# Optimization experiments

Hardware: AMD Instinct MI355X
Metric: run time of the kernel (lower is better)

The kernel has to match this reference:

```python
import jax, jax.numpy as jnp
import numpy as np

N = 131072      # packets
KD = 128        # key_dim
DM = 256        # d_model
HD = 256        # hidden_dim
NC = 1024       # num_compute_nodes
AD = 64         # address_dim
SCALE = 0.1     # residual_scale
ROLE_WRITER = 0


def _ln(x, g, b, eps=1e-5):
    m = jnp.mean(x, axis=-1, keepdims=True)
    v = jnp.mean((x - m) ** 2, axis=-1, keepdims=True)
    return (x - m) * jax.lax.rsqrt(v + eps) * g + b


def setup_inputs() -> dict:
    key = jax.random.key(0)
    ks = jax.random.split(key, 16)
    f32 = jnp.float32

    def w(k, shape):
        return jax.random.normal(k, shape, dtype=f32) * 0.02

    inp = {
        "routing_key": jax.random.normal(ks[0], (N, KD), f32),
        "aux_features": jax.random.normal(ks[1], (N, DM), f32),
        "residual": jax.random.normal(ks[2], (N, DM), f32),
        "role": jax.random.randint(ks[3], (N,), 0, 3, dtype=jnp.int32),
        # input projections
        "Wk": w(ks[4], (KD, HD)), "bk": jnp.zeros((HD,), f32),
        "Wa": w(ks[5], (DM, HD)), "ba": jnp.zeros((HD,), f32),
        "Wr": w(ks[6], (DM, HD)), "br": jnp.zeros((HD,), f32),
        # input layernorm
        "g_in": jnp.ones((HD,), f32), "b_in": jnp.zeros((HD,), f32),
        # backbone layer 0 (Linear + GELU + LN)
        "Wb0": w(ks[7], (HD, HD)), "bb0": jnp.zeros((HD,), f32),
        "g0": jnp.ones((HD,), f32), "beta0": jnp.zeros((HD,), f32),
        # backbone layer 1
        "Wb1": w(ks[8], (HD, HD)), "bb1": jnp.zeros((HD,), f32),
        "g1": jnp.ones((HD,), f32), "beta1": jnp.zeros((HD,), f32),
        # role-specific heads
        "Ww": w(ks[9], (HD, NC)), "bw": jnp.zeros((NC,), f32),
        "Wq": w(ks[10], (HD, NC)), "bq": jnp.zeros((NC,), f32),
        # address head (aux_type == 'address_l2')
        "Wad": w(ks[11], (HD, AD)), "bad": jnp.zeros((AD,), f32),
    }
    return inp


def reference(routing_key, aux_features, residual, role,
              Wk, bk, Wa, ba, Wr, br, g_in, b_in,
              Wb0, bb0, g0, beta0, Wb1, bb1, g1, beta1,
              Ww, bw, Wq, bq, Wad, bad):
    # hidden = key_proj(key) + aux_proj(aux) + scale * residual_proj(residual)
    h = (routing_key @ Wk + bk) + (aux_features @ Wa + ba) \
        + SCALE * (residual @ Wr + br)
    h = _ln(h, g_in, b_in)
    # backbone: [Linear -> GELU -> LN] x layers
    for W, bL, g, be in ((Wb0, bb0, g0, beta0), (Wb1, bb1, g1, beta1)):
        h = _ln(jax.nn.gelu(h @ W + bL, approximate=False), g, be)
    # role-masked head dispatch: writers use writer_head; query + other rows
    # use query_head (matches the torch masked gather/scatter semantics)
    writer = (role == ROLE_WRITER)[:, None]
    logits = jnp.where(writer, h @ Ww + bw, h @ Wq + bq)
    aux_address = h @ Wad + bad
    return logits, h, aux_address
```

## Files before the change

kernel.cpp:

```cpp
#include <hip/hip_runtime.h>
#include <hip/hip_bf16.h>

#define N_PKT 131072
#define KD 128
#define DM 256
#define HDIM 256
#define NCOMP 1024
#define ADIM 64

typedef __attribute__((ext_vector_type(8))) short v8s;
typedef __attribute__((ext_vector_type(4))) float v4f;

__device__ inline unsigned short f2bf(float f) {
  __hip_bfloat16 h = __float2bfloat16(f);
  return *reinterpret_cast<unsigned short*>(&h);
}

__device__ inline float bf2f(unsigned short u) {
  return __uint_as_float(((unsigned)u) << 16);
}

__device__ inline float gelu_f(float x) {
  float x2 = x * x;
  float p = fmaf(x2, 0.10294540f, 2.30208889f);
  float e = __builtin_amdgcn_exp2f(x * p);
  float r = __builtin_amdgcn_rcpf(1.0f + e);
  return x - x * r;
}

struct PrepParams {
  const float *Wk, *Wa, *Wr, *Wb0, *Wb1, *Ww, *Wq, *Wad;
  const float *bk, *ba, *br, *bb0, *bb1;
  const float *g_in, *b_in, *g0, *be0;
  unsigned short* P;
  float* bcomb; float* bb0adj; float* bb1adj;
};

__global__ void prep_kern(PrepParams pp) {
  const int tid = threadIdx.x;
  if (blockIdx.x >= 3264) {
    if (blockIdx.x == 3264) {
      pp.bcomb[tid] = pp.bk[tid] + pp.ba[tid] + 0.1f * pp.br[tid];
    } else {
      const float* vsrc = (blockIdx.x == 3265) ? pp.b_in : pp.be0;
      const float* Wsrc = (blockIdx.x == 3265) ? pp.Wb0 : pp.Wb1;
      const float* badd = (blockIdx.x == 3265) ? pp.bb0 : pp.bb1;
      float* dst = (blockIdx.x == 3265) ? pp.bb0adj : pp.bb1adj;
      float s = badd[tid];
      #pragma unroll 8
      for (int k = 0; k < 256; ++k) s = fmaf(vsrc[k], Wsrc[(long)k * 256 + tid], s);
      dst[tid] = s;
    }
    return;
  }
  long gid = (long)blockIdx.x * 256 + tid;
  int K, Nc; long base; int seg;
  if      (gid < 163840) { K = 640; Nc = 256;  base = 0;      seg = 0; }
  else if (gid < 229376) { K = 256; Nc = 256;  base = 163840; seg = 1; }
  else if (gid < 294912) { K = 256; Nc = 256;  base = 229376; seg = 2; }
  else if (gid < 557056) { K = 256; Nc = 1024; base = 294912; seg = 3; }
  else if (gid < 819200) { K = 256; Nc = 1024; base = 557056; seg = 4; }
  else                   { K = 256; Nc = 64;   base = 819200; seg = 5; }
  long idx = gid - base;
  int j = (int)(idx & 7);
  int l = (int)((idx >> 3) & 63);
  long t = idx >> 9;
  int nKT = K >> 5;
  int kt = (int)(t % nKT), nt = (int)(t / nKT);
  int k = kt * 32 + (l >> 4) * 8 + j;
  int n = nt * 16 + (l & 15);
  float v;
  if (seg == 0) {
    if (k < 128)      v = pp.Wk[(long)k * 256 + n];
    else if (k < 384) v = pp.Wa[(long)(k - 128) * 256 + n];
    else              v = 0.1f * pp.Wr[(long)(k - 384) * 256 + n];
  } else if (seg == 1) v = pp.g_in[k] * pp.Wb0[(long)k * 256 + n];
  else if (seg == 2)   v = pp.g0[k] * pp.Wb1[(long)k * 256 + n];
  else if (seg == 3)   v = pp.Ww[(long)k * Nc + n];
  else if (seg == 4)   v = pp.Wq[(long)k * Nc + n];
  else                 v = pp.Wad[(long)k * Nc + n];
  pp.P[gid] = f2bf(v);
}

template<int COLS>
__device__ inline void stage_tile(const float* __restrict__ src, long R0,
                                  const int* __restrict__ rows,
                                  unsigned short (&tile)[64][264], int tid) {
  constexpr int C4 = COLS / 4;
  constexpr int NV = 64 * C4;
  #pragma unroll
  for (int i = 0; i < NV / 256; ++i) {
    int idx = tid + i * 256;
    int r = idx / C4;
    int c4 = idx % C4;
    float4 v = *(reinterpret_cast<const float4*>(src + (R0 + rows[r]) * (long)COLS) + c4);
    unsigned long long pk = (unsigned long long)f2bf(v.x)
                          | ((unsigned long long)f2bf(v.y) << 16)
                          | ((unsigned long long)f2bf(v.z) << 32)
                          | ((unsigned long long)f2bf(v.w) << 48);
    *reinterpret_cast<unsigned long long*>(&tile[r][c4 * 4]) = pk;
  }
}

template<int NKT, int KTOFF, int KSTRIDE>
__device__ inline void gemm_acc(const unsigned short* __restrict__ Wp, int nt0,
                                const unsigned short (&tile)[64][264], int lane,
                                v4f (&acc)[4][4]) {
  const int lr = lane & 15, lg = lane >> 4;
  #pragma unroll
  for (int kt = 0; kt < NKT; ++kt) {
    v8s b[4];
    #pragma unroll
    for (int nf = 0; nf < 4; ++nf)
      b[nf] = *reinterpret_cast<const v8s*>(
          Wp + (((long)(nt0 + nf) * KSTRIDE + KTOFF + kt) * 64 + lane) * 8);
    #pragma unroll
    for (int m = 0; m < 4; ++m) {
      v8s a = *reinterpret_cast<const v8s*>(&tile[m * 16 + lr][kt * 32 + lg * 8]);
      #pragma unroll
      for (int nf = 0; nf < 4; ++nf)
        acc[m][nf] = __builtin_amdgcn_mfma_f32_16x16x32_bf16(a, b[nf], acc[m][nf], 0, 0, 0);
    }
  }
}

__device__ inline void init_acc(v4f (&acc)[4][4], const float* __restrict__ bias,
                                int colbase, int lr) {
  float bv[4];
  #pragma unroll
  for (int nf = 0; nf < 4; ++nf) bv[nf] = bias[colbase + nf * 16 + lr];
  #pragma unroll
  for (int m = 0; m < 4; ++m)
    #pragma unroll
    for (int nf = 0; nf < 4; ++nf)
      acc[m][nf] = (v4f){bv[nf], bv[nf], bv[nf], bv[nf]};
}

template<bool GELU, bool AFFINE>
__device__ inline void ln_stage(v4f (&acc)[4][4], int wave, int lane,
                                const float* __restrict__ gamma, const float* __restrict__ beta,
                                unsigned short (&tile)[64][264], float (&stats)[2][4][64]) {
  const int lr = lane & 15, lg = lane >> 4;
  if (GELU) {
    #pragma unroll
    for (int m = 0; m < 4; ++m)
      #pragma unroll
      for (int nf = 0; nf < 4; ++nf)
        #pragma unroll
        for (int r = 0; r < 4; ++r)
          acc[m][nf][r] = gelu_f(acc[m][nf][r]);
  }
  float s[4][4], q[4][4];
  #pragma unroll
  for (int m = 0; m < 4; ++m)
    #pragma unroll
    for (int r = 0; r < 4; ++r) {
      float t = 0.f, t2 = 0.f;
      #pragma unroll
      for (int nf = 0; nf < 4; ++nf) { float v = acc[m][nf][r]; t += v; t2 = fmaf(v, v, t2); }
      s[m][r] = t; q[m][r] = t2;
    }
  #pragma unroll
  for (int off = 1; off < 16; off <<= 1)
    #pragma unroll
    for (int m = 0; m < 4; ++m)
      #pragma unroll
      for (int r = 0; r < 4; ++r) {
        s[m][r] += __shfl_xor(s[m][r], off);
        q[m][r] += __shfl_xor(q[m][r], off);
      }
  if (lr == 0) {
    #pragma unroll
    for (int m = 0; m < 4; ++m)
      #pragma unroll
      for (int r = 0; r < 4; ++r) {
        int row = m * 16 + lg * 4 + r;
        stats[0][wave][row] = s[m][r];
        stats[1][wave][row] = q[m][r];
      }
  }
  __syncthreads();
  float gv[4], bv[4];
  if (AFFINE) {
    #pragma unroll
    for (int nf = 0; nf < 4; ++nf) {
      int c = wave * 64 + nf * 16 + lr;
      gv[nf] = gamma[c]; bv[nf] = beta[c];
    }
  }
  #pragma unroll
  for (int m = 0; m < 4; ++m)
    #pragma unroll
    for (int r = 0; r < 4; ++r) {
      int row = m * 16 + lg * 4 + r;
      float S = stats[0][0][row] + stats[0][1][row] + stats[0][2][row] + stats[0][3][row];
      float Q = stats[1][0][row] + stats[1][1][row] + stats[1][2][row] + stats[1][3][row];
      float mean = S * (1.0f / 256.0f);
      float var  = Q * (1.0f / 256.0f) - mean * mean;
      float rstd = rsqrtf(var + 1e-5f);
      #pragma unroll
      for (int nf = 0; nf < 4; ++nf) {
        int c = wave * 64 + nf * 16 + lr;
        float z = (acc[m][nf][r] - mean) * rstd;
        float y = AFFINE ? fmaf(z, gv[nf], bv[nf]) : z;
        tile[row][c] = f2bf(y);
      }
    }
  __syncthreads();
}

struct MegaParams {
  const float* key; const float* aux; const float* res; const int* role;
  const unsigned short* pWcat; const unsigned short* pWb0; const unsigned short* pWb1;
  const unsigned short* pWad; const unsigned short* pWw; const unsigned short* pWq;
  const float* bcomb; const float* bb0adj; const float* bb1adj;
  const float* g1; const float* be1; const float* bad;
  const float* bw; const float* bq;
  float* out_logits; float* out_h; float* out_aux;
};

__global__ __launch_bounds__(256, 3) void mega_kern(MegaParams p) {
  __shared__ alignas(16) unsigned short tile[64][264];
  __shared__ float stats[2][4][64];
  __shared__ alignas(16) float stage[4][16][68];
  __shared__ int rows[64];
  __shared__ int nwS;

  const int tid = threadIdx.x;
  const int lane = tid & 63;
  const int wave = tid >> 6;
  const int lr = lane & 15;
  const int lg = lane >> 4;
  const long R0 = (long)blockIdx.x * 64;
  const int nt0 = wave * 4;

  if (tid < 64) {
    int w = (p.role[R0 + tid] == 0) ? 1 : 0;
    unsigned long long mw = __ballot(w != 0);
    unsigned long long below = (tid == 0) ? 0ull : (~0ull >> (64 - tid));
    int nw = __popcll(mw);
    int pos = w ? __popcll(mw & below) : nw + __popcll((~mw) & below);
    rows[pos] = tid;
    if (tid == 0) nwS = nw;
  }
  __syncthreads();
  const int nw = nwS;

  v4f acc[4][4];

  init_acc(acc, p.bcomb, wave * 64, lr);
  stage_tile<KD>(p.key, R0, rows, tile, tid);
  __syncthreads();
  gemm_acc<4, 0, 20>(p.pWcat, nt0, tile, lane, acc);
  __syncthreads();
  stage_tile<DM>(p.aux, R0, rows, tile, tid);
  __syncthreads();
  gemm_acc<8, 4, 20>(p.pWcat, nt0, tile, lane, acc);
  __syncthreads();
  stage_tile<DM>(p.res, R0, rows, tile, tid);
  __syncthreads();
  gemm_acc<8, 12, 20>(p.pWcat, nt0, tile, lane, acc);
  ln_stage<false, false>(acc, wave, lane, nullptr, nullptr, tile, stats);

  init_acc(acc, p.bb0adj, wave * 64, lr);
  gemm_acc<8, 0, 8>(p.pWb0, nt0, tile, lane, acc);
  ln_stage<true, false>(acc, wave, lane, nullptr, nullptr, tile, stats);

  init_acc(acc, p.bb1adj, wave * 64, lr);
  gemm_acc<8, 0, 8>(p.pWb1, nt0, tile, lane, acc);
  ln_stage<true, true>(acc, wave, lane, p.g1, p.be1, tile, stats);

  #pragma unroll
  for (int i = 0; i < 16; ++i) {
    int slot = wave * 16 + i;
    unsigned long long t4 = *reinterpret_cast<const unsigned long long*>(&tile[slot][lane * 4]);
    v4f v;
    v[0] = bf2f((unsigned short)(t4 & 0xffff));
    v[1] = bf2f((unsigned short)((t4 >> 16) & 0xffff));
    v[2] = bf2f((unsigned short)((t4 >> 32) & 0xffff));
    v[3] = bf2f((unsigned short)((t4 >> 48) & 0xffff));
    *reinterpret_cast<v4f*>(p.out_h + (R0 + rows[slot]) * HDIM + lane * 4) = v;
  }

  {
    float (*astage)[68] = reinterpret_cast<float(*)[68]>(&stage[0][0][0]);
    v4f a4[4];
    float bv = p.bad[wave * 16 + lr];
    #pragma unroll
    for (int m = 0; m < 4; ++m) a4[m] = (v4f){bv, bv, bv, bv};
    #pragma unroll
    for (int kt = 0; kt < 8; ++kt) {
      v8s b = *reinterpret_cast<const v8s*>(p.pWad + (((long)wave * 8 + kt) * 64 + lane) * 8);
      #pragma unroll
      for (int m = 0; m < 4; ++m) {
        v8s am = *reinterpret_cast<const v8s*>(&tile[m * 16 + lr][kt * 32 + lg * 8]);
        a4[m] = __builtin_amdgcn_mfma_f32_16x16x32_bf16(am, b, a4[m], 0, 0, 0);
      }
    }
    #pragma unroll
    for (int m = 0; m < 4; ++m)
      #pragma unroll
      for (int r = 0; r < 4; ++r)
        astage[m * 16 + lg * 4 + r][wave * 16 + lr] = a4[m][r];
    __syncthreads();
    #pragma unroll
    for (int k = 0; k < 4; ++k) {
      int idx = tid + k * 256;
      int slot = idx >> 4;
      int c4 = idx & 15;
      v4f v = *reinterpret_cast<const v4f*>(&astage[slot][c4 * 4]);
      *reinterpret_cast<v4f*>(p.out_aux + (R0 + rows[slot]) * ADIM + c4 * 4) = v;
    }
    __syncthreads();
  }

  const int rr = lane >> 3;
  const int ce = lane & 7;
  #pragma unroll 1
  for (int hsel = 0; hsel < 2; ++hsel) {
    const unsigned short* Wp = hsel == 0 ? p.pWw : p.pWq;
    const float* bias = hsel == 0 ? p.bw : p.bq;
    bool needm[4];
    #pragma unroll
    for (int m = 0; m < 4; ++m)
      needm[m] = (hsel == 0) ? (m * 16 < nw) : ((m + 1) * 16 > nw);
    #pragma unroll 1
    for (int c = 0; c < 4; ++c) {
      const int nth = wave * 16 + c * 4;
      v4f hacc[4][4];
      #pragma unroll
      for (int nf = 0; nf < 4; ++nf) {
        v4f bv = *reinterpret_cast<const v4f*>(bias + (nth + nf) * 16 + lg * 4);
        #pragma unroll
        for (int m = 0; m < 4; ++m) hacc[m][nf] = bv;
      }
      v8s wcur[4], wnxt[4];
      #pragma unroll
      for (int nf = 0; nf < 4; ++nf)
        wcur[nf] = *reinterpret_cast<const v8s*>(Wp + (((long)(nth + nf) * 8 + 0) * 64 + lane) * 8);
      #pragma unroll
      for (int kt = 0; kt < 8; ++kt) {
        if (kt < 7) {
          #pragma unroll
          for (int nf = 0; nf < 4; ++nf)
            wnxt[nf] = *reinterpret_cast<const v8s*>(Wp + (((long)(nth + nf) * 8 + kt + 1) * 64 + lane) * 8);
        }
        #pragma unroll
        for (int m = 0; m < 4; ++m) {
          if (!needm[m]) continue;
          v8s a = *reinterpret_cast<const v8s*>(&tile[m * 16 + lr][kt * 32 + lg * 8]);
          #pragma unroll
          for (int nf = 0; nf < 4; ++nf)
            hacc[m][nf] = __builtin_amdgcn_mfma_f32_16x16x32_bf16(wcur[nf], a, hacc[m][nf], 0, 0, 0);
        }
        if (kt < 7) {
          #pragma unroll
          for (int nf = 0; nf < 4; ++nf) wcur[nf] = wnxt[nf];
        }
      }
      #pragma unroll
      for (int m = 0; m < 4; ++m) {
        if (!needm[m]) continue;
        #pragma unroll
        for (int nf = 0; nf < 4; ++nf)
          *reinterpret_cast<v4f*>(&stage[wave][lr][nf * 16 + lg * 4]) = hacc[m][nf];
        __builtin_amdgcn_sched_barrier(0);
        #pragma unroll
        for (int rh = 0; rh < 2; ++rh) {
          int slot = m * 16 + rh * 8 + rr;
          bool doit = (hsel == 0) ? (slot < nw) : (slot >= nw);
          int ridx = rows[slot];
          #pragma unroll
          for (int ch = 0; ch < 2; ++ch) {
            v4f v = *reinterpret_cast<const v4f*>(&stage[wave][rh * 8 + rr][ch * 32 + ce * 4]);
            if (doit)
              *reinterpret_cast<v4f*>(p.out_logits + (R0 + ridx) * NCOMP
                                      + nth * 16 + ch * 32 + ce * 4) = v;
          }
        }
        __builtin_amdgcn_sched_barrier(0);
      }
    }
  }
}

extern "C" void kernel_launch(void* const* d_in, const int* in_sizes, int n_in,
                              void* d_out, int out_size, void* d_ws, size_t ws_size,
                              hipStream_t stream) {
  const float* key  = (const float*)d_in[0];
  const float* aux  = (const float*)d_in[1];
  const float* res  = (const float*)d_in[2];
  const int*   role = (const int*)d_in[3];
  const float* Wk = (const float*)d_in[4];   const float* bk = (const float*)d_in[5];
  const float* Wa = (const float*)d_in[6];   const float* ba = (const float*)d_in[7];
  const float* Wr = (const float*)d_in[8];   const float* br = (const float*)d_in[9];
  const float* g_in = (const float*)d_in[10]; const float* b_in = (const float*)d_in[11];
  const float* Wb0 = (const float*)d_in[12]; const float* bb0 = (const float*)d_in[13];
  const float* g0 = (const float*)d_in[14];  const float* be0 = (const float*)d_in[15];
  const float* Wb1 = (const float*)d_in[16]; const float* bb1 = (const float*)d_in[17];
  const float* g1 = (const float*)d_in[18];  const float* be1 = (const float*)d_in[19];
  const float* Ww = (const float*)d_in[20];  const float* bw = (const float*)d_in[21];
  const float* Wq = (const float*)d_in[22];  const float* bq = (const float*)d_in[23];
  const float* Wad = (const float*)d_in[24]; const float* bad = (const float*)d_in[25];

  unsigned short* wsp = (unsigned short*)d_ws;
  unsigned short* pWcat = wsp + 0;
  unsigned short* pWb0  = wsp + 163840;
  unsigned short* pWb1  = wsp + 229376;
  unsigned short* pWw   = wsp + 294912;
  unsigned short* pWq   = wsp + 557056;
  unsigned short* pWad  = wsp + 819200;
  char* wsb = (char*)d_ws;
  float* bcomb  = (float*)(wsb + 1671168);
  float* bb0adj = (float*)(wsb + 1672192);
  float* bb1adj = (float*)(wsb + 1673216);

  PrepParams pp;
  pp.Wk = Wk; pp.Wa = Wa; pp.Wr = Wr; pp.Wb0 = Wb0; pp.Wb1 = Wb1;
  pp.Ww = Ww; pp.Wq = Wq; pp.Wad = Wad;
  pp.bk = bk; pp.ba = ba; pp.br = br; pp.bb0 = bb0; pp.bb1 = bb1;
  pp.g_in = g_in; pp.b_in = b_in; pp.g0 = g0; pp.be0 = be0;
  pp.P = wsp; pp.bcomb = bcomb; pp.bb0adj = bb0adj; pp.bb1adj = bb1adj;
  prep_kern<<<3267, 256, 0, stream>>>(pp);

  float* out = (float*)d_out;
  MegaParams P;
  P.key = key; P.aux = aux; P.res = res; P.role = role;
  P.pWcat = pWcat; P.pWb0 = pWb0; P.pWb1 = pWb1; P.pWad = pWad;
  P.pWw = pWw; P.pWq = pWq;
  P.bcomb = bcomb; P.bb0adj = bb0adj; P.bb1adj = bb1adj;
  P.g1 = g1; P.be1 = be1; P.bad = bad; P.bw = bw; P.bq = bq;
  P.out_logits = out;
  P.out_h = out + (size_t)N_PKT * NCOMP;
  P.out_aux = out + (size_t)N_PKT * (NCOMP + HDIM);
  mega_kern<<<N_PKT / 64, 256, 0, stream>>>(P);
}
```

Before: 360.8 us.

## Repartition backbone GEMMs so each wave owns 16 full rows, removing block barriers

The input-projection and backbone stages now give each wave 16 complete rows across all 256 output columns, instead of splitting the columns across waves. LayerNorm statistics can then be reduced within a wave by shuffles alone, which removes the shared-memory stats array and every __syncthreads between staging, GEMM and LN. Each wave now streams the full weight matrix from global/L2 for its own 16 rows, so weight traffic per block rises by 4x. The A-fragment reuse per B load also drops (one A fragment feeds 16 MFMAs, but each B fragment is used only once).

```diff
diff --git a/kernel.cpp b/kernel.cpp
--- a/kernel.cpp
+++ b/kernel.cpp
@@ -83,15 +83,14 @@
 }
 
 template<int COLS>
-__device__ inline void stage_tile(const float* __restrict__ src, long R0,
-                                  const int* __restrict__ rows,
-                                  unsigned short (&tile)[64][264], int tid) {
+__device__ inline void stage_rows_w(const float* __restrict__ src, long R0,
+                                    const int* __restrict__ rows,
+                                    unsigned short (&tile)[64][264], int wrow0, int lane) {
   constexpr int C4 = COLS / 4;
-  constexpr int NV = 64 * C4;
-  #pragma unroll
-  for (int i = 0; i < NV / 256; ++i) {
-    int idx = tid + i * 256;
-    int r = idx / C4;
+  #pragma unroll
+  for (int j = 0; j < 16 * C4 / 64; ++j) {
+    int idx = lane + j * 64;
+    int r = wrow0 + idx / C4;
     int c4 = idx % C4;
     float4 v = *(reinterpret_cast<const float4*>(src + (R0 + rows[r]) * (long)COLS) + c4);
     unsigned long long pk = (unsigned long long)f2bf(v.x)
@@ -103,110 +102,75 @@
 }
 
 template<int NKT, int KTOFF, int KSTRIDE>
-__device__ inline void gemm_acc(const unsigned short* __restrict__ Wp, int nt0,
-                                const unsigned short (&tile)[64][264], int lane,
-                                v4f (&acc)[4][4]) {
+__device__ inline void gemm_w(const unsigned short* __restrict__ Wp,
+                              const unsigned short (&tile)[64][264],
+                              int wrow0, int lane, v4f (&acc)[16]) {
   const int lr = lane & 15, lg = lane >> 4;
   #pragma unroll
   for (int kt = 0; kt < NKT; ++kt) {
-    v8s b[4];
-    #pragma unroll
-    for (int nf = 0; nf < 4; ++nf)
-      b[nf] = *reinterpret_cast<const v8s*>(
-          Wp + (((long)(nt0 + nf) * KSTRIDE + KTOFF + kt) * 64 + lane) * 8);
-    #pragma unroll
-    for (int m = 0; m < 4; ++m) {
-      v8s a = *reinterpret_cast<const v8s*>(&tile[m * 16 + lr][kt * 32 + lg * 8]);
-      #pragma unroll
-      for (int nf = 0; nf < 4; ++nf)
-        acc[m][nf] = __builtin_amdgcn_mfma_f32_16x16x32_bf16(a, b[nf], acc[m][nf], 0, 0, 0);
-    }
-  }
-}
-
-__device__ inline void init_acc(v4f (&acc)[4][4], const float* __restrict__ bias,
-                                int colbase, int lr) {
-  float bv[4];
-  #pragma unroll
-  for (int nf = 0; nf < 4; ++nf) bv[nf] = bias[colbase + nf * 16 + lr];
-  #pragma unroll
-  for (int m = 0; m < 4; ++m)
-    #pragma unroll
-    for (int nf = 0; nf < 4; ++nf)
-      acc[m][nf] = (v4f){bv[nf], bv[nf], bv[nf], bv[nf]};
+    v8s a = *reinterpret_cast<const v8s*>(&tile[wrow0 + lr][kt * 32 + lg * 8]);
+    #pragma unroll
+    for (int nt = 0; nt < 16; ++nt) {
+      v8s b = *reinterpret_cast<const v8s*>(
+          Wp + (((long)nt * KSTRIDE + KTOFF + kt) * 64 + lane) * 8);
+      acc[nt] = __builtin_amdgcn_mfma_f32_16x16x32_bf16(a, b, acc[nt], 0, 0, 0);
+    }
+  }
+}
+
+__device__ inline void init_acc_w(v4f (&acc)[16], const float* __restrict__ bias, int lr) {
+  #pragma unroll
+  for (int nt = 0; nt < 16; ++nt) {
+    float bv = bias[nt * 16 + lr];
+    acc[nt] = (v4f){bv, bv, bv, bv};
+  }
 }
 
 template<bool GELU, bool AFFINE>
-__device__ inline void ln_stage(v4f (&acc)[4][4], int wave, int lane,
-                                const float* __restrict__ gamma, const float* __restrict__ beta,
-                                unsigned short (&tile)[64][264], float (&stats)[2][4][64]) {
+__device__ inline void ln_w(v4f (&acc)[16], int lane,
+                            const float* __restrict__ gamma, const float* __restrict__ beta,
+                            unsigned short (&tile)[64][264], int wrow0) {
   const int lr = lane & 15, lg = lane >> 4;
   if (GELU) {
     #pragma unroll
-    for (int m = 0; m < 4; ++m)
-      #pragma unroll
-      for (int nf = 0; nf < 4; ++nf)
-        #pragma unroll
-        for (int r = 0; r < 4; ++r)
-          acc[m][nf][r] = gelu_f(acc[m][nf][r]);
-  }
-  float s[4][4], q[4][4];
-  #pragma unroll
-  for (int m = 0; m < 4; ++m)
+    for (int nt = 0; nt < 16; ++nt)
+      #pragma unroll
+      for (int r = 0; r < 4; ++r)
+        acc[nt][r] = gelu_f(acc[nt][r]);
+  }
+  float s[4], q[4];
+  #pragma unroll
+  for (int r = 0; r < 4; ++r) {
+    float t = 0.f, t2 = 0.f;
+    #pragma unroll
+    for (int nt = 0; nt < 16; ++nt) { float v = acc[nt][r]; t += v; t2 = fmaf(v, v, t2); }
+    s[r] = t; q[r] = t2;
+  }
+  #pragma unroll
+  for (int off = 1; off < 16; off <<= 1)
     #pragma unroll
     for (int r = 0; r < 4; ++r) {
-      float t = 0.f, t2 = 0.f;
-      #pragma unroll
-      for (int nf = 0; nf < 4; ++nf) { float v = acc[m][nf][r]; t += v; t2 = fmaf(v, v, t2); }
-      s[m][r] = t; q[m][r] = t2;
-    }
-  #pragma unroll
-  for (int off = 1; off < 16; off <<= 1)
-    #pragma unroll
-    for (int m = 0; m < 4; ++m)
-      #pragma unroll
-      for (int r = 0; r < 4; ++r) {
-        s[m][r] += __shfl_xor(s[m][r], off);
-        q[m][r] += __shfl_xor(q[m][r], off);
-      }
-  if (lr == 0) {
-    #pragma unroll
-    for (int m = 0; m < 4; ++m)
-      #pragma unroll
-      for (int r = 0; r < 4; ++r) {
-        int row = m * 16 + lg * 4 + r;
-        stats[0][wave][row] = s[m][r];
-        stats[1][wave][row] = q[m][r];
-      }
-  }
-  __syncthreads();
-  float gv[4], bv[4];
-  if (AFFINE) {
-    #pragma unroll
-    for (int nf = 0; nf < 4; ++nf) {
-      int c = wave * 64 + nf * 16 + lr;
-      gv[nf] = gamma[c]; bv[nf] = beta[c];
-    }
-  }
-  #pragma unroll
-  for (int m = 0; m < 4; ++m)
+      s[r] += __shfl_xor(s[r], off);
+      q[r] += __shfl_xor(q[r], off);
+    }
+  float mean[4], rstd[4];
+  #pragma unroll
+  for (int r = 0; r < 4; ++r) {
+    mean[r] = s[r] * (1.0f / 256.0f);
+    float var = q[r] * (1.0f / 256.0f) - mean[r] * mean[r];
+    rstd[r] = rsqrtf(var + 1e-5f);
+  }
+  #pragma unroll
+  for (int nt = 0; nt < 16; ++nt) {
+    float gv = 1.f, bv = 0.f;
+    if (AFFINE) { gv = gamma[nt * 16 + lr]; bv = beta[nt * 16 + lr]; }
     #pragma unroll
     for (int r = 0; r < 4; ++r) {
-      int row = m * 16 + lg * 4 + r;
-      float S = stats[0][0][row] + stats[0][1][row] + stats[0][2][row] + stats[0][3][row];
-      float Q = stats[1][0][row] + stats[1][1][row] + stats[1][2][row] + stats[1][3][row];
-      float mean = S * (1.0f / 256.0f);
-      float var  = Q * (1.0f / 256.0f) - mean * mean;
-      float rstd = rsqrtf(var + 1e-5f);
-      #pragma unroll
-      for (int nf = 0; nf < 4; ++nf) {
-        int c = wave * 64 + nf * 16 + lr;
-        float z = (acc[m][nf][r] - mean) * rstd;
-        float y = AFFINE ? fmaf(z, gv[nf], bv[nf]) : z;
-        tile[row][c] = f2bf(y);
-      }
-    }
-  __syncthreads();
+      float z = (acc[nt][r] - mean[r]) * rstd[r];
+      float y = AFFINE ? fmaf(z, gv, bv) : z;
+      tile[wrow0 + lg * 4 + r][nt * 16 + lr] = f2bf(y);
+    }
+  }
 }
 
 struct MegaParams {
@@ -221,7 +185,6 @@
 
 __global__ __launch_bounds__(256, 3) void mega_kern(MegaParams p) {
   __shared__ alignas(16) unsigned short tile[64][264];
-  __shared__ float stats[2][4][64];
   __shared__ alignas(16) float stage[4][16][68];
   __shared__ int rows[64];
   __shared__ int nwS;
@@ -232,47 +195,42 @@
   const int lr = lane & 15;
   const int lg = lane >> 4;
   const long R0 = (long)blockIdx.x * 64;
-  const int nt0 = wave * 4;
+  const int wrow0 = wave * 16;
 
   if (tid < 64) {
     int w = (p.role[R0 + tid] == 0) ? 1 : 0;
     unsigned long long mw = __ballot(w != 0);
     unsigned long long below = (tid == 0) ? 0ull : (~0ull >> (64 - tid));
-    int nw = __popcll(mw);
-    int pos = w ? __popcll(mw & below) : nw + __popcll((~mw) & below);
+    int nwv = __popcll(mw);
+    int pos = w ? __popcll(mw & below) : nwv + __popcll((~mw) & below);
     rows[pos] = tid;
-    if (tid == 0) nwS = nw;
+    if (tid == 0) nwS = nwv;
   }
   __syncthreads();
   const int nw = nwS;
 
-  v4f acc[4][4];
-
-  init_acc(acc, p.bcomb, wave * 64, lr);
-  stage_tile<KD>(p.key, R0, rows, tile, tid);
-  __syncthreads();
-  gemm_acc<4, 0, 20>(p.pWcat, nt0, tile, lane, acc);
-  __syncthreads();
-  stage_tile<DM>(p.aux, R0, rows, tile, tid);
-  __syncthreads();
-  gemm_acc<8, 4, 20>(p.pWcat, nt0, tile, lane, acc);
-  __syncthreads();
-  stage_tile<DM>(p.res, R0, rows, tile, tid);
-  __syncthreads();
-  gemm_acc<8, 12, 20>(p.pWcat, nt0, tile, lane, acc);
-  ln_stage<false, false>(acc, wave, lane, nullptr, nullptr, tile, stats);
-
-  init_acc(acc, p.bb0adj, wave * 64, lr);
-  gemm_acc<8, 0, 8>(p.pWb0, nt0, tile, lane, acc);
-  ln_stage<true, false>(acc, wave, lane, nullptr, nullptr, tile, stats);
-
-  init_acc(acc, p.bb1adj, wave * 64, lr);
-  gemm_acc<8, 0, 8>(p.pWb1, nt0, tile, lane, acc);
-  ln_stage<true, true>(acc, wave, lane, p.g1, p.be1, tile, stats);
+  v4f acc[16];
+
+  init_acc_w(acc, p.bcomb, lr);
+  stage_rows_w<KD>(p.key, R0, rows, tile, wrow0, lane);
+  gemm_w<4, 0, 20>(p.pWcat, tile, wrow0, lane, acc);
+  stage_rows_w<DM>(p.aux, R0, rows, tile, wrow0, lane);
+  gemm_w<8, 4, 20>(p.pWcat, tile, wrow0, lane, acc);
+  stage_rows_w<DM>(p.res, R0, rows, tile, wrow0, lane);
+  gemm_w<8, 12, 20>(p.pWcat, tile, wrow0, lane, acc);
+  ln_w<false, false>(acc, lane, nullptr, nullptr, tile, wrow0);
+
+  init_acc_w(acc, p.bb0adj, lr);
+  gemm_w<8, 0, 8>(p.pWb0, tile, wrow0, lane, acc);
+  ln_w<true, false>(acc, lane, nullptr, nullptr, tile, wrow0);
+
+  init_acc_w(acc, p.bb1adj, lr);
+  gemm_w<8, 0, 8>(p.pWb1, tile, wrow0, lane, acc);
+  ln_w<true, true>(acc, lane, p.g1, p.be1, tile, wrow0);
 
   #pragma unroll
   for (int i = 0; i < 16; ++i) {
-    int slot = wave * 16 + i;
+    int slot = wrow0 + i;
     unsigned long long t4 = *reinterpret_cast<const unsigned long long*>(&tile[slot][lane * 4]);
     v4f v;
     v[0] = bf2f((unsigned short)(t4 & 0xffff));
@@ -281,6 +239,8 @@
     v[3] = bf2f((unsigned short)((t4 >> 48) & 0xffff));
     *reinterpret_cast<v4f*>(p.out_h + (R0 + rows[slot]) * HDIM + lane * 4) = v;
   }
+
+  __syncthreads();
 
   {
     float (*astage)[68] = reinterpret_cast<float(*)[68]>(&stage[0][0][0]);
```

Measured after the change: 848.5 us. 135% more time.

## Prefetch next input tile into registers while MFMA runs on current tile

Applied to the files above, without the earlier changes.

Replaces the synchronous stage_tile calls with register prefetching. Global loads of the aux and residual rows are issued before the GEMM on the previous tile, then packed to bf16 and stored to shared memory after it. This is meant to hide global memory latency behind matrix-core work. It costs 64 extra VGPRs for the float4 buffer, which may lower occupancy or cause spills alongside the 64-register accumulator.

```diff
diff --git a/kernel.cpp b/kernel.cpp
--- a/kernel.cpp
+++ b/kernel.cpp
@@ -26,6 +26,13 @@
   float e = __builtin_amdgcn_exp2f(x * p);
   float r = __builtin_amdgcn_rcpf(1.0f + e);
   return x - x * r;
+}
+
+__device__ inline unsigned long long pack4(float4 v) {
+  return (unsigned long long)f2bf(v.x)
+       | ((unsigned long long)f2bf(v.y) << 16)
+       | ((unsigned long long)f2bf(v.z) << 32)
+       | ((unsigned long long)f2bf(v.w) << 48);
 }
 
 struct PrepParams {
@@ -82,26 +89,6 @@
   pp.P[gid] = f2bf(v);
 }
 
-template<int COLS>
-__device__ inline void stage_tile(const float* __restrict__ src, long R0,
-                                  const int* __restrict__ rows,
-                                  unsigned short (&tile)[64][264], int tid) {
-  constexpr int C4 = COLS / 4;
-  constexpr int NV = 64 * C4;
-  #pragma unroll
-  for (int i = 0; i < NV / 256; ++i) {
-    int idx = tid + i * 256;
-    int r = idx / C4;
-    int c4 = idx % C4;
-    float4 v = *(reinterpret_cast<const float4*>(src + (R0 + rows[r]) * (long)COLS) + c4);
-    unsigned long long pk = (unsigned long long)f2bf(v.x)
-                          | ((unsigned long long)f2bf(v.y) << 16)
-                          | ((unsigned long long)f2bf(v.z) << 32)
-                          | ((unsigned long long)f2bf(v.w) << 48);
-    *reinterpret_cast<unsigned long long*>(&tile[r][c4 * 4]) = pk;
-  }
-}
-
 template<int NKT, int KTOFF, int KSTRIDE>
 __device__ inline void gemm_acc(const unsigned short* __restrict__ Wp, int nt0,
                                 const unsigned short (&tile)[64][264], int lane,
@@ -249,15 +236,43 @@
   v4f acc[4][4];
 
   init_acc(acc, p.bcomb, wave * 64, lr);
-  stage_tile<KD>(p.key, R0, rows, tile, tid);
-  __syncthreads();
+  float4 pre[16];
+  #pragma unroll
+  for (int i = 0; i < 8; ++i) {
+    int idx = tid + i * 256;
+    pre[i] = *(reinterpret_cast<const float4*>(p.key + (R0 + rows[idx >> 5]) * (long)KD) + (idx & 31));
+  }
+  #pragma unroll
+  for (int i = 0; i < 8; ++i) {
+    int idx = tid + i * 256;
+    *reinterpret_cast<unsigned long long*>(&tile[idx >> 5][(idx & 31) * 4]) = pack4(pre[i]);
+  }
+  __syncthreads();
+  #pragma unroll
+  for (int i = 0; i < 16; ++i) {
+    int idx = tid + i * 256;
+    pre[i] = *(reinterpret_cast<const float4*>(p.aux + (R0 + rows[idx >> 6]) * (long)DM) + (idx & 63));
+  }
   gemm_acc<4, 0, 20>(p.pWcat, nt0, tile, lane, acc);
   __syncthreads();
-  stage_tile<DM>(p.aux, R0, rows, tile, tid);
-  __syncthreads();
+  #pragma unroll
+  for (int i = 0; i < 16; ++i) {
+    int idx = tid + i * 256;
+    *reinterpret_cast<unsigned long long*>(&tile[idx >> 6][(idx & 63) * 4]) = pack4(pre[i]);
+  }
+  __syncthreads();
+  #pragma unroll
+  for (int i = 0; i < 16; ++i) {
+    int idx = tid + i * 256;
+    pre[i] = *(reinterpret_cast<const float4*>(p.res + (R0 + rows[idx >> 6]) * (long)DM) + (idx & 63));
+  }
   gemm_acc<8, 4, 20>(p.pWcat, nt0, tile, lane, acc);
   __syncthreads();
-  stage_tile<DM>(p.res, R0, rows, tile, tid);
+  #pragma unroll
+  for (int i = 0; i < 16; ++i) {
+    int idx = tid + i * 256;
+    *reinterpret_cast<unsigned long long*>(&tile[idx >> 6][(idx & 63) * 4]) = pack4(pre[i]);
+  }
   __syncthreads();
   gemm_acc<8, 12, 20>(p.pWcat, nt0, tile, lane, acc);
   ln_stage<false, false>(acc, wave, lane, nullptr, nullptr, tile, stats);
```

New measurement: 433.6 us. 20.2% more time.
